# Performance work log

Measured on AMD Instinct MI355X. Metric: run time of the kernel, lower is better.

The kernel has to match this reference:

```python
import jax, jax.numpy as jnp
import numpy as np

X_DIM, Y_DIM = 5, 2
H1, H2 = 560, 40
GRU_H = 5 * (X_DIM * X_DIM + Y_DIM * Y_DIM)  # 145
N_GRU = 2


def _gru_cell(x, h, Wih, Whh, bih, bhh):
    # PyTorch GRUCell math. Wih:(3H,in), Whh:(3H,H)
    gi = Wih @ x + bih
    gh = Whh @ h + bhh
    i_r, i_z, i_n = jnp.split(gi, 3)
    h_r, h_z, h_n = jnp.split(gh, 3)
    r = jax.nn.sigmoid(i_r + h_r)
    z = jax.nn.sigmoid(i_z + h_z)
    n = jnp.tanh(i_n + r * h_n)
    return (1.0 - z) * n + z * h


def setup_inputs() -> dict:
    key = jax.random.key(0)
    ks = jax.random.split(key, 20)
    s = lambda k, sh, fan: (jax.random.uniform(k, sh, jnp.float32, -1.0, 1.0) / np.sqrt(fan))
    inp = {
        "state_inno": jax.random.normal(ks[0], (X_DIM,), jnp.float32),
        "obs_inno": jax.random.normal(ks[1], (Y_DIM,), jnp.float32),
        "diff_state": jax.random.normal(ks[2], (X_DIM,), jnp.float32),
        "diff_obs": jax.random.normal(ks[3], (Y_DIM,), jnp.float32),
        # l1: Linear(14 -> H1)
        "W1": s(ks[4], (H1, 2 * X_DIM + 2 * Y_DIM), 2 * X_DIM + 2 * Y_DIM),
        "b1": s(ks[5], (H1,), 2 * X_DIM + 2 * Y_DIM),
        # GRU layer 0: input H1 -> GRU_H
        "Wih0": s(ks[6], (3 * GRU_H, H1), GRU_H),
        "Whh0": s(ks[7], (3 * GRU_H, GRU_H), GRU_H),
        "bih0": s(ks[8], (3 * GRU_H,), GRU_H),
        "bhh0": s(ks[9], (3 * GRU_H,), GRU_H),
        # GRU layer 1: input GRU_H -> GRU_H
        "Wih1": s(ks[10], (3 * GRU_H, GRU_H), GRU_H),
        "Whh1": s(ks[11], (3 * GRU_H, GRU_H), GRU_H),
        "bih1": s(ks[12], (3 * GRU_H,), GRU_H),
        "bhh1": s(ks[13], (3 * GRU_H,), GRU_H),
        # l2: Linear(GRU_H -> H2) -> ReLU -> Linear(H2 -> x_dim*y_dim)
        "W2a": s(ks[14], (H2, GRU_H), GRU_H),
        "b2a": s(ks[15], (H2,), GRU_H),
        "W2b": s(ks[16], (X_DIM * Y_DIM, H2), H2),
        "b2b": s(ks[17], (X_DIM * Y_DIM,), H2),
        # hidden state hn: (n_layers, batch=1, GRU_H) -> squeeze batch
        "hn": jax.random.normal(ks[18], (N_GRU, GRU_H), jnp.float32),
    }
    return inp


def reference(state_inno, obs_inno, diff_state, diff_obs,
              W1, b1, Wih0, Whh0, bih0, bhh0, Wih1, Whh1, bih1, bhh1,
              W2a, b2a, W2b, b2b, hn):
    x = jnp.concatenate([state_inno, obs_inno, diff_state, diff_obs])  # (14,)
    l1_out = jax.nn.relu(W1 @ x + b1)  # (H1,)
    h0 = _gru_cell(l1_out, hn[0], Wih0, Whh0, bih0, bhh0)  # (GRU_H,)
    h1 = _gru_cell(h0, hn[1], Wih1, Whh1, bih1, bhh1)       # (GRU_H,)
    l2_hidden = jax.nn.relu(W2a @ h1 + b2a)
    l2_out = W2b @ l2_hidden + b2b  # (x_dim*y_dim,)
    kalman_gain = l2_out.reshape(X_DIM, Y_DIM)
    return kalman_gain
```

## Files before the change

### kernel.cpp

```cpp
#include <hip/hip_runtime.h>

#define X_DIM 5
#define Y_DIM 2
#define H1 560
#define H2 40
#define GRUH 145
#define G3 435
#define NB_H0 37
#define NB_GH1 109
#define NB_K2 37

__device__ __forceinline__ float wave_reduce(float v) {
#pragma unroll
    for (int off = 32; off > 0; off >>= 1)
        v += __shfl_xor(v, off, 64);
    return v;
}

__device__ __forceinline__ float sigmoidf_(float x) {
    return 1.0f / (1.0f + __expf(-x));
}

__device__ __forceinline__ float dot4(float4 a, float4 b) {
    return fmaf(a.x, b.x, fmaf(a.y, b.y, fmaf(a.z, b.z, a.w * b.w)));
}

__global__ __launch_bounds__(256) void k1_gru0(
    const float* __restrict__ si, const float* __restrict__ oi,
    const float* __restrict__ dst, const float* __restrict__ dob,
    const float* __restrict__ W1, const float* __restrict__ b1,
    const float* __restrict__ Wih0, const float* __restrict__ Whh0,
    const float* __restrict__ bih0, const float* __restrict__ bhh0,
    const float* __restrict__ Whh1, const float* __restrict__ bhh1,
    const float* __restrict__ hn,
    unsigned* __restrict__ ctr,
    float* __restrict__ h0g, float* __restrict__ gh1g)
{
    const int tid = threadIdx.x;
    const int wid = tid >> 6, lane = tid & 63;
    const bool t3 = (lane < 17);

    if (blockIdx.x < NB_H0) {
        __shared__ __align__(16) float sl1[H1];
        const int e   = blockIdx.x * 4 + wid;
        const bool act = (e < GRUH);
        const int ee  = act ? e : (GRUH - 1);

        const float* wr0 = Whh0 + (ee           ) * GRUH;
        const float* wr1 = Whh0 + (ee +   GRUH  ) * GRUH;
        const float* wr2 = Whh0 + (ee + 2 * GRUH) * GRUH;
        const float h_a = hn[lane], h_b = hn[lane + 64], h_c = t3 ? hn[lane + 128] : 0.f;
        const float w00 = wr0[lane], w01 = wr0[lane + 64], w02 = t3 ? wr0[lane + 128] : 0.f;
        const float w10 = wr1[lane], w11 = wr1[lane + 64], w12 = t3 ? wr1[lane + 128] : 0.f;
        const float w20 = wr2[lane], w21 = wr2[lane + 64], w22 = t3 ? wr2[lane + 128] : 0.f;

        const bool f3 = (lane < 12);
        const float4 z4 = make_float4(0.f, 0.f, 0.f, 0.f);
        const float4* p0 = reinterpret_cast<const float4*>(Wih0 + (ee           ) * H1);
        const float4* p1 = reinterpret_cast<const float4*>(Wih0 + (ee +   GRUH  ) * H1);
        const float4* p2 = reinterpret_cast<const float4*>(Wih0 + (ee + 2 * GRUH) * H1);
        const float4 q00 = p0[lane], q01 = p0[lane + 64], q02 = f3 ? p0[lane + 128] : z4;
        const float4 q10 = p1[lane], q11 = p1[lane + 64], q12 = f3 ? p1[lane + 128] : z4;
        const float4 q20 = p2[lane], q21 = p2[lane + 64], q22 = f3 ? p2[lane + 128] : z4;

        const float bi0 = bih0[ee], bi1 = bih0[ee + GRUH], bi2 = bih0[ee + 2 * GRUH];
        const float bh0 = bhh0[ee], bh1 = bhh0[ee + GRUH], bh2 = bhh0[ee + 2 * GRUH];
        const float hne = hn[ee];

        float x[14];
#pragma unroll
        for (int k = 0; k < 5; ++k) x[k] = si[k];
        x[5] = oi[0]; x[6] = oi[1];
#pragma unroll
        for (int k = 0; k < 5; ++k) x[7 + k] = dst[k];
        x[12] = dob[0]; x[13] = dob[1];

        for (int j = tid; j < H1; j += 256) {
            float a = b1[j];
            const float* wp = W1 + j * 14;
#pragma unroll
            for (int k = 0; k < 14; ++k) a = fmaf(wp[k], x[k], a);
            sl1[j] = fmaxf(a, 0.0f);
        }

        float a3 = fmaf(w00, h_a, fmaf(w01, h_b, w02 * h_c));
        float a4 = fmaf(w10, h_a, fmaf(w11, h_b, w12 * h_c));
        float a5 = fmaf(w20, h_a, fmaf(w21, h_b, w22 * h_c));

        __syncthreads();

        const float4 s0 = *reinterpret_cast<const float4*>(&sl1[4 * lane]);
        const float4 s1 = *reinterpret_cast<const float4*>(&sl1[4 * (lane + 64)]);
        const float4 s2 = f3 ? *reinterpret_cast<const float4*>(&sl1[4 * (lane + 128)]) : z4;
        float a0 = dot4(q00, s0) + dot4(q01, s1) + dot4(q02, s2);
        float a1 = dot4(q10, s0) + dot4(q11, s1) + dot4(q12, s2);
        float a2 = dot4(q20, s0) + dot4(q21, s1) + dot4(q22, s2);

        a0 = wave_reduce(a0); a1 = wave_reduce(a1); a2 = wave_reduce(a2);
        a3 = wave_reduce(a3); a4 = wave_reduce(a4); a5 = wave_reduce(a5);
        if (lane == 0 && act) {
            const float r = sigmoidf_(a0 + bi0 + a3 + bh0);
            const float z = sigmoidf_(a1 + bi1 + a4 + bh1);
            const float n = tanhf   (a2 + bi2 + r * (a5 + bh2));
            h0g[e] = (1.0f - z) * n + z * hne;
        }
    } else {
        if (blockIdx.x == NB_H0 && tid == 0)
            __hip_atomic_store(ctr, 0u, __ATOMIC_RELAXED, __HIP_MEMORY_SCOPE_AGENT);
        const int r   = (blockIdx.x - NB_H0) * 4 + wid;
        const bool act = (r < G3);
        const int rr  = act ? r : (G3 - 1);
        const float* rp = Whh1 + rr * GRUH;
        const float wa = rp[lane], wb = rp[lane + 64], wc = t3 ? rp[lane + 128] : 0.f;
        const float ha = hn[GRUH + lane], hb = hn[GRUH + lane + 64],
                    hc = t3 ? hn[GRUH + lane + 128] : 0.f;
        const float bb = bhh1[rr];
        float a = fmaf(wa, ha, fmaf(wb, hb, wc * hc));
        a = wave_reduce(a);
        if (lane == 0 && act) gh1g[r] = a + bb;
    }
}

__global__ __launch_bounds__(256) void k2_gru1_head(
    const float* __restrict__ Wih1, const float* __restrict__ bih1,
    const float* __restrict__ W2a, const float* __restrict__ b2a,
    const float* __restrict__ W2b, const float* __restrict__ b2b,
    const float* __restrict__ hn,
    const float* __restrict__ h0g, const float* __restrict__ gh1g,
    unsigned* __restrict__ ctr,
    float* __restrict__ h1g, float* __restrict__ out)
{
    __shared__ float sh1[GRUH];
    __shared__ float sl2h[H2];
    __shared__ unsigned slast;

    const int tid = threadIdx.x;
    const int wid = tid >> 6, lane = tid & 63;
    const bool t3 = (lane < 17);
    const int e   = blockIdx.x * 4 + wid;
    const bool act = (e < GRUH);
    const int ee  = act ? e : (GRUH - 1);

    const float* r0 = Wih1 + (ee           ) * GRUH;
    const float* r1 = Wih1 + (ee +   GRUH  ) * GRUH;
    const float* r2 = Wih1 + (ee + 2 * GRUH) * GRUH;
    const float w0a = r0[lane], w0b = r0[lane + 64], w0c = t3 ? r0[lane + 128] : 0.f;
    const float w1a = r1[lane], w1b = r1[lane + 64], w1c = t3 ? r1[lane + 128] : 0.f;
    const float w2a = r2[lane], w2b = r2[lane + 64], w2c = t3 ? r2[lane + 128] : 0.f;
    const float g0 = gh1g[ee], g1 = gh1g[ee + GRUH], g2 = gh1g[ee + 2 * GRUH];
    const float bi0 = bih1[ee], bi1 = bih1[ee + GRUH], bi2 = bih1[ee + 2 * GRUH];
    const float hne = hn[GRUH + ee];

    const float x0 = h0g[lane], x1 = h0g[lane + 64], x2 = t3 ? h0g[lane + 128] : 0.f;

    float c0 = fmaf(w0a, x0, fmaf(w0b, x1, w0c * x2));
    float c1 = fmaf(w1a, x0, fmaf(w1b, x1, w1c * x2));
    float c2 = fmaf(w2a, x0, fmaf(w2b, x1, w2c * x2));
    c0 = wave_reduce(c0); c1 = wave_reduce(c1); c2 = wave_reduce(c2);
    if (lane == 0 && act) {
        const float r = sigmoidf_(c0 + bi0 + g0);
        const float z = sigmoidf_(c1 + bi1 + g1);
        const float n = tanhf   (c2 + bi2 + r * g2);
        const float v = (1.0f - z) * n + z * hne;
        __hip_atomic_store(&h1g[e], v, __ATOMIC_RELEASE, __HIP_MEMORY_SCOPE_AGENT);
    }
    __syncthreads();
    if (tid == 0) {
        const unsigned old =
            __hip_atomic_fetch_add(ctr, 1u, __ATOMIC_ACQ_REL, __HIP_MEMORY_SCOPE_AGENT);
        slast = (old == NB_K2 - 1u) ? 1u : 0u;
    }

    float wa[10][3];
    const int rbase = wid * 10;
#pragma unroll
    for (int m = 0; m < 10; ++m) {
        const float* rp = W2a + (rbase + m) * GRUH;
        wa[m][0] = rp[lane];
        wa[m][1] = rp[lane + 64];
        wa[m][2] = t3 ? rp[lane + 128] : 0.f;
    }
    float ba[10];
#pragma unroll
    for (int m = 0; m < 10; ++m) ba[m] = b2a[rbase + m];
    float wb2[H2], bb2 = 0.f;
    if (tid < X_DIM * Y_DIM) {
        const float* rp = W2b + tid * H2;
#pragma unroll
        for (int k = 0; k < H2; ++k) wb2[k] = rp[k];
        bb2 = b2b[tid];
    }

    __syncthreads();
    if (!slast) return;

    for (int j = tid; j < GRUH; j += 256)
        sh1[j] = __hip_atomic_load(&h1g[j], __ATOMIC_ACQUIRE, __HIP_MEMORY_SCOPE_AGENT);
    __syncthreads();

    const float ya = sh1[lane], yb = sh1[lane + 64], yc = t3 ? sh1[lane + 128] : 0.f;
#pragma unroll
    for (int m = 0; m < 10; ++m) {
        float a = fmaf(wa[m][0], ya, fmaf(wa[m][1], yb, wa[m][2] * yc));
        a = wave_reduce(a);
        if (lane == 0) sl2h[rbase + m] = fmaxf(a + ba[m], 0.0f);
    }
    __syncthreads();
    if (tid < X_DIM * Y_DIM) {
        float a = bb2;
#pragma unroll
        for (int k = 0; k < H2; ++k) a = fmaf(wb2[k], sl2h[k], a);
        out[tid] = a;
    }
}

extern "C" void kernel_launch(void* const* d_in, const int* in_sizes, int n_in,
                              void* d_out, int out_size, void* d_ws, size_t ws_size,
                              hipStream_t stream) {
    const float* si   = (const float*)d_in[0];
    const float* oi   = (const float*)d_in[1];
    const float* dst  = (const float*)d_in[2];
    const float* dob  = (const float*)d_in[3];
    const float* W1   = (const float*)d_in[4];
    const float* b1   = (const float*)d_in[5];
    const float* Wih0 = (const float*)d_in[6];
    const float* Whh0 = (const float*)d_in[7];
    const float* bih0 = (const float*)d_in[8];
    const float* bhh0 = (const float*)d_in[9];
    const float* Wih1 = (const float*)d_in[10];
    const float* Whh1 = (const float*)d_in[11];
    const float* bih1 = (const float*)d_in[12];
    const float* bhh1 = (const float*)d_in[13];
    const float* W2a  = (const float*)d_in[14];
    const float* b2a  = (const float*)d_in[15];
    const float* W2b  = (const float*)d_in[16];
    const float* b2b  = (const float*)d_in[17];
    const float* hn   = (const float*)d_in[18];

    float* ws = (float*)d_ws;
    unsigned* ctr = (unsigned*)d_ws;
    float* h0g  = ws + 64;
    float* gh1g = ws + 64 + 256;
    float* h1g  = ws + 64 + 256 + 512;

    hipLaunchKernelGGL(k1_gru0, dim3(NB_H0 + NB_GH1), dim3(256), 0, stream,
                       si, oi, dst, dob, W1, b1, Wih0, Whh0, bih0, bhh0,
                       Whh1, bhh1, hn, ctr, h0g, gh1g);
    hipLaunchKernelGGL(k2_gru1_head, dim3(NB_K2), dim3(256), 0, stream,
                       Wih1, bih1, W2a, b2a, W2b, b2b, hn, h0g, gh1g,
                       ctr, h1g, (float*)d_out);
}
```

Before: 16.33 us.

## Move GRU layer-1 hidden matvec into second kernel and vectorize l1 layer

The Whh1·hn[1] matvec moves out of the first kernel's 109 extra blocks and into the second kernel, where each wave computes its own three hidden-gate rows beside the input-gate rows. That drops the gh1 workspace round trip and shrinks the first grid to 37 blocks. The l1 linear layer is also rewritten to load each W1 row as float2 pairs with three fully unrolled rows per thread, and the input vector is loaded with vector loads. The second kernel now issues more global loads per wave before its reduction, which could lengthen its critical path.

```diff
diff --git a/kernel.cpp b/kernel.cpp
--- a/kernel.cpp
+++ b/kernel.cpp
@@ -6,8 +6,7 @@
 #define H2 40
 #define GRUH 145
 #define G3 435
-#define NB_H0 37
-#define NB_GH1 109
+#define NB_K1 37
 #define NB_K2 37
 
 __device__ __forceinline__ float wave_reduce(float v) {
@@ -16,11 +15,7 @@
         v += __shfl_xor(v, off, 64);
     return v;
 }
-
-__device__ __forceinline__ float sigmoidf_(float x) {
-    return 1.0f / (1.0f + __expf(-x));
-}
-
+__device__ __forceinline__ float sigmoidf_(float x) { return 1.0f / (1.0f + __expf(-x)); }
 __device__ __forceinline__ float dot4(float4 a, float4 b) {
     return fmaf(a.x, b.x, fmaf(a.y, b.y, fmaf(a.z, b.z, a.w * b.w)));
 }
@@ -31,102 +26,98 @@
     const float* __restrict__ W1, const float* __restrict__ b1,
     const float* __restrict__ Wih0, const float* __restrict__ Whh0,
     const float* __restrict__ bih0, const float* __restrict__ bhh0,
-    const float* __restrict__ Whh1, const float* __restrict__ bhh1,
     const float* __restrict__ hn,
     unsigned* __restrict__ ctr,
-    float* __restrict__ h0g, float* __restrict__ gh1g)
+    float* __restrict__ h0g)
 {
+    __shared__ __align__(16) float sl1[H1];
+
     const int tid = threadIdx.x;
     const int wid = tid >> 6, lane = tid & 63;
     const bool t3 = (lane < 17);
-
-    if (blockIdx.x < NB_H0) {
-        __shared__ __align__(16) float sl1[H1];
-        const int e   = blockIdx.x * 4 + wid;
-        const bool act = (e < GRUH);
-        const int ee  = act ? e : (GRUH - 1);
-
-        const float* wr0 = Whh0 + (ee           ) * GRUH;
-        const float* wr1 = Whh0 + (ee +   GRUH  ) * GRUH;
-        const float* wr2 = Whh0 + (ee + 2 * GRUH) * GRUH;
-        const float h_a = hn[lane], h_b = hn[lane + 64], h_c = t3 ? hn[lane + 128] : 0.f;
-        const float w00 = wr0[lane], w01 = wr0[lane + 64], w02 = t3 ? wr0[lane + 128] : 0.f;
-        const float w10 = wr1[lane], w11 = wr1[lane + 64], w12 = t3 ? wr1[lane + 128] : 0.f;
-        const float w20 = wr2[lane], w21 = wr2[lane + 64], w22 = t3 ? wr2[lane + 128] : 0.f;
-
-        const bool f3 = (lane < 12);
-        const float4 z4 = make_float4(0.f, 0.f, 0.f, 0.f);
-        const float4* p0 = reinterpret_cast<const float4*>(Wih0 + (ee           ) * H1);
-        const float4* p1 = reinterpret_cast<const float4*>(Wih0 + (ee +   GRUH  ) * H1);
-        const float4* p2 = reinterpret_cast<const float4*>(Wih0 + (ee + 2 * GRUH) * H1);
-        const float4 q00 = p0[lane], q01 = p0[lane + 64], q02 = f3 ? p0[lane + 128] : z4;
-        const float4 q10 = p1[lane], q11 = p1[lane + 64], q12 = f3 ? p1[lane + 128] : z4;
-        const float4 q20 = p2[lane], q21 = p2[lane + 64], q22 = f3 ? p2[lane + 128] : z4;
-
-        const float bi0 = bih0[ee], bi1 = bih0[ee + GRUH], bi2 = bih0[ee + 2 * GRUH];
-        const float bh0 = bhh0[ee], bh1 = bhh0[ee + GRUH], bh2 = bhh0[ee + 2 * GRUH];
-        const float hne = hn[ee];
-
-        float x[14];
-#pragma unroll
-        for (int k = 0; k < 5; ++k) x[k] = si[k];
-        x[5] = oi[0]; x[6] = oi[1];
-#pragma unroll
-        for (int k = 0; k < 5; ++k) x[7 + k] = dst[k];
-        x[12] = dob[0]; x[13] = dob[1];
-
-        for (int j = tid; j < H1; j += 256) {
-            float a = b1[j];
-            const float* wp = W1 + j * 14;
-#pragma unroll
-            for (int k = 0; k < 14; ++k) a = fmaf(wp[k], x[k], a);
-            sl1[j] = fmaxf(a, 0.0f);
-        }
-
-        float a3 = fmaf(w00, h_a, fmaf(w01, h_b, w02 * h_c));
-        float a4 = fmaf(w10, h_a, fmaf(w11, h_b, w12 * h_c));
-        float a5 = fmaf(w20, h_a, fmaf(w21, h_b, w22 * h_c));
-
-        __syncthreads();
-
-        const float4 s0 = *reinterpret_cast<const float4*>(&sl1[4 * lane]);
-        const float4 s1 = *reinterpret_cast<const float4*>(&sl1[4 * (lane + 64)]);
-        const float4 s2 = f3 ? *reinterpret_cast<const float4*>(&sl1[4 * (lane + 128)]) : z4;
-        float a0 = dot4(q00, s0) + dot4(q01, s1) + dot4(q02, s2);
-        float a1 = dot4(q10, s0) + dot4(q11, s1) + dot4(q12, s2);
-        float a2 = dot4(q20, s0) + dot4(q21, s1) + dot4(q22, s2);
-
-        a0 = wave_reduce(a0); a1 = wave_reduce(a1); a2 = wave_reduce(a2);
-        a3 = wave_reduce(a3); a4 = wave_reduce(a4); a5 = wave_reduce(a5);
-        if (lane == 0 && act) {
-            const float r = sigmoidf_(a0 + bi0 + a3 + bh0);
-            const float z = sigmoidf_(a1 + bi1 + a4 + bh1);
-            const float n = tanhf   (a2 + bi2 + r * (a5 + bh2));
-            h0g[e] = (1.0f - z) * n + z * hne;
-        }
-    } else {
-        if (blockIdx.x == NB_H0 && tid == 0)
-            __hip_atomic_store(ctr, 0u, __ATOMIC_RELAXED, __HIP_MEMORY_SCOPE_AGENT);
-        const int r   = (blockIdx.x - NB_H0) * 4 + wid;
-        const bool act = (r < G3);
-        const int rr  = act ? r : (G3 - 1);
-        const float* rp = Whh1 + rr * GRUH;
-        const float wa = rp[lane], wb = rp[lane + 64], wc = t3 ? rp[lane + 128] : 0.f;
-        const float ha = hn[GRUH + lane], hb = hn[GRUH + lane + 64],
-                    hc = t3 ? hn[GRUH + lane + 128] : 0.f;
-        const float bb = bhh1[rr];
-        float a = fmaf(wa, ha, fmaf(wb, hb, wc * hc));
-        a = wave_reduce(a);
-        if (lane == 0 && act) gh1g[r] = a + bb;
+    const bool f3 = (lane < 12);
+    const float4 z4 = make_float4(0.f, 0.f, 0.f, 0.f);
+
+    if (blockIdx.x == 0 && tid == 0)
+        __hip_atomic_store(ctr, 0u, __ATOMIC_RELAXED, __HIP_MEMORY_SCOPE_AGENT);
+
+    const int e   = blockIdx.x * 4 + wid;
+    const bool act = (e < GRUH);
+    const int ee  = act ? e : (GRUH - 1);
+
+    const float4* p0 = reinterpret_cast<const float4*>(Wih0 + (ee           ) * H1);
+    const float4* p1 = reinterpret_cast<const float4*>(Wih0 + (ee +   GRUH  ) * H1);
+    const float4* p2 = reinterpret_cast<const float4*>(Wih0 + (ee + 2 * GRUH) * H1);
+    const float4 q00 = p0[lane], q01 = p0[lane + 64], q02 = f3 ? p0[lane + 128] : z4;
+    const float4 q10 = p1[lane], q11 = p1[lane + 64], q12 = f3 ? p1[lane + 128] : z4;
+    const float4 q20 = p2[lane], q21 = p2[lane + 64], q22 = f3 ? p2[lane + 128] : z4;
+    const float* wr0 = Whh0 + (ee           ) * GRUH;
+    const float* wr1 = Whh0 + (ee +   GRUH  ) * GRUH;
+    const float* wr2 = Whh0 + (ee + 2 * GRUH) * GRUH;
+    const float w00 = wr0[lane], w01 = wr0[lane + 64], w02 = t3 ? wr0[lane + 128] : 0.f;
+    const float w10 = wr1[lane], w11 = wr1[lane + 64], w12 = t3 ? wr1[lane + 128] : 0.f;
+    const float w20 = wr2[lane], w21 = wr2[lane + 64], w22 = t3 ? wr2[lane + 128] : 0.f;
+    const float ha = hn[lane], hb = hn[lane + 64], hc = t3 ? hn[lane + 128] : 0.f;
+    const float bi0 = bih0[ee], bi1 = bih0[ee + GRUH], bi2 = bih0[ee + 2 * GRUH];
+    const float bh0 = bhh0[ee], bh1 = bhh0[ee + GRUH], bh2 = bhh0[ee + 2 * GRUH];
+    const float hne = hn[ee];
+
+    const float4 s4 = *reinterpret_cast<const float4*>(si);
+    const float  s5 = si[4];
+    const float2 o2 = *reinterpret_cast<const float2*>(oi);
+    const float4 d4 = *reinterpret_cast<const float4*>(dst);
+    const float  d5 = dst[4];
+    const float2 e2 = *reinterpret_cast<const float2*>(dob);
+    float x[14] = { s4.x, s4.y, s4.z, s4.w, s5, o2.x, o2.y,
+                    d4.x, d4.y, d4.z, d4.w, d5, e2.x, e2.y };
+
+    const int j0 = tid, j1 = tid + 256, j2 = tid + 512;
+    const bool has2 = (j2 < H1);
+    float2 A[7], B[7], C[7];
+    const float2* w1p0 = reinterpret_cast<const float2*>(W1 + j0 * 14);
+    const float2* w1p1 = reinterpret_cast<const float2*>(W1 + j1 * 14);
+    const float2* w1p2 = reinterpret_cast<const float2*>(W1 + (has2 ? j2 : j0) * 14);
+#pragma unroll
+    for (int k = 0; k < 7; ++k) { A[k] = w1p0[k]; B[k] = w1p1[k]; C[k] = w1p2[k]; }
+    const float bb0 = b1[j0], bb1_ = b1[j1], bb2_ = b1[has2 ? j2 : j0];
+    float a0_ = bb0, a1_ = bb1_, a2_ = bb2_;
+#pragma unroll
+    for (int k = 0; k < 7; ++k) {
+        a0_ = fmaf(A[k].x, x[2 * k], fmaf(A[k].y, x[2 * k + 1], a0_));
+        a1_ = fmaf(B[k].x, x[2 * k], fmaf(B[k].y, x[2 * k + 1], a1_));
+        a2_ = fmaf(C[k].x, x[2 * k], fmaf(C[k].y, x[2 * k + 1], a2_));
+    }
+    sl1[j0] = fmaxf(a0_, 0.0f);
+    sl1[j1] = fmaxf(a1_, 0.0f);
+    if (has2) sl1[j2] = fmaxf(a2_, 0.0f);
+    __syncthreads();
+
+    const float4 s0 = *reinterpret_cast<const float4*>(&sl1[4 * lane]);
+    const float4 s1 = *reinterpret_cast<const float4*>(&sl1[4 * (lane + 64)]);
+    const float4 s2 = f3 ? *reinterpret_cast<const float4*>(&sl1[4 * (lane + 128)]) : z4;
+    float a0 = dot4(q00, s0) + dot4(q01, s1) + dot4(q02, s2);
+    float a1 = dot4(q10, s0) + dot4(q11, s1) + dot4(q12, s2);
+    float a2 = dot4(q20, s0) + dot4(q21, s1) + dot4(q22, s2);
+    float a3 = fmaf(w00, ha, fmaf(w01, hb, w02 * hc));
+    float a4 = fmaf(w10, ha, fmaf(w11, hb, w12 * hc));
+    float a5 = fmaf(w20, ha, fmaf(w21, hb, w22 * hc));
+    a0 = wave_reduce(a0); a1 = wave_reduce(a1); a2 = wave_reduce(a2);
+    a3 = wave_reduce(a3); a4 = wave_reduce(a4); a5 = wave_reduce(a5);
+    if (lane == 0 && act) {
+        const float r = sigmoidf_(a0 + bi0 + a3 + bh0);
+        const float z = sigmoidf_(a1 + bi1 + a4 + bh1);
+        const float n = tanhf   (a2 + bi2 + r * (a5 + bh2));
+        h0g[e] = (1.0f - z) * n + z * hne;
     }
 }
 
 __global__ __launch_bounds__(256) void k2_gru1_head(
-    const float* __restrict__ Wih1, const float* __restrict__ bih1,
+    const float* __restrict__ Wih1, const float* __restrict__ Whh1,
+    const float* __restrict__ bih1, const float* __restrict__ bhh1,
     const float* __restrict__ W2a, const float* __restrict__ b2a,
     const float* __restrict__ W2b, const float* __restrict__ b2b,
     const float* __restrict__ hn,
-    const float* __restrict__ h0g, const float* __restrict__ gh1g,
+    const float* __restrict__ h0g,
     unsigned* __restrict__ ctr,
     float* __restrict__ h1g, float* __restrict__ out)
 {
@@ -147,21 +138,32 @@
     const float w0a = r0[lane], w0b = r0[lane + 64], w0c = t3 ? r0[lane + 128] : 0.f;
     const float w1a = r1[lane], w1b = r1[lane + 64], w1c = t3 ? r1[lane + 128] : 0.f;
     const float w2a = r2[lane], w2b = r2[lane + 64], w2c = t3 ? r2[lane + 128] : 0.f;
-    const float g0 = gh1g[ee], g1 = gh1g[ee + GRUH], g2 = gh1g[ee + 2 * GRUH];
+    const float* u0 = Whh1 + (ee           ) * GRUH;
+    const float* u1 = Whh1 + (ee +   GRUH  ) * GRUH;
+    const float* u2 = Whh1 + (ee + 2 * GRUH) * GRUH;
+    const float v0a = u0[lane], v0b = u0[lane + 64], v0c = t3 ? u0[lane + 128] : 0.f;
+    const float v1a = u1[lane], v1b = u1[lane + 64], v1c = t3 ? u1[lane + 128] : 0.f;
+    const float v2a = u2[lane], v2b = u2[lane + 64], v2c = t3 ? u2[lane + 128] : 0.f;
     const float bi0 = bih1[ee], bi1 = bih1[ee + GRUH], bi2 = bih1[ee + 2 * GRUH];
-    const float hne = hn[GRUH + ee];
-
+    const float bh0 = bhh1[ee], bh1 = bhh1[ee + GRUH], bh2 = bhh1[ee + 2 * GRUH];
+    const float ya = hn[GRUH + lane], yb = hn[GRUH + lane + 64],
+                yc = t3 ? hn[GRUH + lane + 128] : 0.f;
+    const float hn1e = hn[GRUH + ee];
     const float x0 = h0g[lane], x1 = h0g[lane + 64], x2 = t3 ? h0g[lane + 128] : 0.f;
 
     float c0 = fmaf(w0a, x0, fmaf(w0b, x1, w0c * x2));
     float c1 = fmaf(w1a, x0, fmaf(w1b, x1, w1c * x2));
     float c2 = fmaf(w2a, x0, fmaf(w2b, x1, w2c * x2));
+    float d0 = fmaf(v0a, ya, fmaf(v0b, yb, v0c * yc));
+    float d1 = fmaf(v1a, ya, fmaf(v1b, yb, v1c * yc));
+    float d2 = fmaf(v2a, ya, fmaf(v2b, yb, v2c * yc));
     c0 = wave_reduce(c0); c1 = wave_reduce(c1); c2 = wave_reduce(c2);
+    d0 = wave_reduce(d0); d1 = wave_reduce(d1); d2 = wave_reduce(d2);
     if (lane == 0 && act) {
-        const float r = sigmoidf_(c0 + bi0 + g0);
-        const float z = sigmoidf_(c1 + bi1 + g1);
-        const float n = tanhf   (c2 + bi2 + r * g2);
-        const float v = (1.0f - z) * n + z * hne;
+        const float r = sigmoidf_(c0 + bi0 + d0 + bh0);
+        const float z = sigmoidf_(c1 + bi1 + d1 + bh1);
+        const float n = tanhf   (c2 + bi2 + r * (d2 + bh2));
+        const float v = (1.0f - z) * n + z * hn1e;
         __hip_atomic_store(&h1g[e], v, __ATOMIC_RELEASE, __HIP_MEMORY_SCOPE_AGENT);
     }
     __syncthreads();
@@ -198,10 +200,10 @@
         sh1[j] = __hip_atomic_load(&h1g[j], __ATOMIC_ACQUIRE, __HIP_MEMORY_SCOPE_AGENT);
     __syncthreads();
 
-    const float ya = sh1[lane], yb = sh1[lane + 64], yc = t3 ? sh1[lane + 128] : 0.f;
+    const float za = sh1[lane], zb = sh1[lane + 64], zc = t3 ? sh1[lane + 128] : 0.f;
 #pragma unroll
     for (int m = 0; m < 10; ++m) {
-        float a = fmaf(wa[m][0], ya, fmaf(wa[m][1], yb, wa[m][2] * yc));
+        float a = fmaf(wa[m][0], za, fmaf(wa[m][1], zb, wa[m][2] * zc));
         a = wave_reduce(a);
         if (lane == 0) sl2h[rbase + m] = fmaxf(a + ba[m], 0.0f);
     }
@@ -239,14 +241,13 @@
 
     float* ws = (float*)d_ws;
     unsigned* ctr = (unsigned*)d_ws;
-    float* h0g  = ws + 64;
-    float* gh1g = ws + 64 + 256;
-    float* h1g  = ws + 64 + 256 + 512;
-
-    hipLaunchKernelGGL(k1_gru0, dim3(NB_H0 + NB_GH1), dim3(256), 0, stream,
+    float* h0g = ws + 64;
+    float* h1g = ws + 64 + 256;
+
+    hipLaunchKernelGGL(k1_gru0, dim3(NB_K1), dim3(256), 0, stream,
                        si, oi, dst, dob, W1, b1, Wih0, Whh0, bih0, bhh0,
-                       Whh1, bhh1, hn, ctr, h0g, gh1g);
+                       hn, ctr, h0g);
     hipLaunchKernelGGL(k2_gru1_head, dim3(NB_K2), dim3(256), 0, stream,
-                       Wih1, bih1, W2a, b2a, W2b, b2b, hn, h0g, gh1g,
-                       ctr, h1g, (float*)d_out);
-}
+                       Wih1, Whh1, bih1, bhh1, W2a, b2a, W2b, b2b, hn,
+                       h0g, ctr, h1g, (float*)d_out);
+}
```

After: 16.85 us. 1.03x slower.
